# Optimization experiments

Measured on AMD Instinct MI355X. Metric: run time of the kernel, lower is better.

## Reference

```python
import jax, jax.numpy as jnp
import numpy as np

D_MODEL = 1024
NUM_HEADS = 16
D_K = D_MODEL // NUM_HEADS
D_FF = 4096
EPS = 1e-5


def setup_inputs() -> dict:
    key = jax.random.key(0)
    ks = jax.random.split(key, 16)
    B, S = 2, 2048
    s_attn = 1.0 / np.sqrt(D_MODEL)
    s_ff1 = 1.0 / np.sqrt(D_MODEL)
    s_ff2 = 1.0 / np.sqrt(D_FF)
    return {
        "x": jax.random.normal(ks[0], (B, S, D_MODEL), jnp.float32),
        "Wq": jax.random.normal(ks[1], (D_MODEL, D_MODEL), jnp.float32) * s_attn,
        "bq": jnp.zeros((D_MODEL,), jnp.float32),
        "Wk": jax.random.normal(ks[2], (D_MODEL, D_MODEL), jnp.float32) * s_attn,
        "bk": jnp.zeros((D_MODEL,), jnp.float32),
        "Wv": jax.random.normal(ks[3], (D_MODEL, D_MODEL), jnp.float32) * s_attn,
        "bv": jnp.zeros((D_MODEL,), jnp.float32),
        "Wo": jax.random.normal(ks[4], (D_MODEL, D_MODEL), jnp.float32) * s_attn,
        "bo": jnp.zeros((D_MODEL,), jnp.float32),
        "W1": jax.random.normal(ks[5], (D_MODEL, D_FF), jnp.float32) * s_ff1,
        "b1": jnp.zeros((D_FF,), jnp.float32),
        "W2": jax.random.normal(ks[6], (D_FF, D_MODEL), jnp.float32) * s_ff2,
        "b2": jnp.zeros((D_MODEL,), jnp.float32),
        "g1": jnp.ones((D_MODEL,), jnp.float32),
        "be1": jnp.zeros((D_MODEL,), jnp.float32),
        "g2": jnp.ones((D_MODEL,), jnp.float32),
        "be2": jnp.zeros((D_MODEL,), jnp.float32),
    }


def _layernorm(x, g, b):
    m = jnp.mean(x, axis=-1, keepdims=True)
    v = jnp.mean(jnp.square(x - m), axis=-1, keepdims=True)
    return (x - m) * jax.lax.rsqrt(v + EPS) * g + b


def _split_heads(x, B, S):
    # (B, S, D) -> (B, H, S, d_k)
    return x.reshape(B, S, NUM_HEADS, D_K).transpose(0, 2, 1, 3)


def reference(x, Wq, bq, Wk, bk, Wv, bv, Wo, bo, W1, b1, W2, b2, g1, be1, g2, be2):
    B, S, _ = x.shape
    Q = _split_heads(x @ Wq + bq, B, S)
    K = _split_heads(x @ Wk + bk, B, S)
    V = _split_heads(x @ Wv + bv, B, S)
    scores = jnp.einsum("bhqd,bhkd->bhqk", Q, K) / np.sqrt(D_K).astype(np.float32)
    attn = jax.nn.softmax(scores, axis=-1)  # dropout is identity (p=0 / eval)
    ctx = jnp.einsum("bhqk,bhkd->bhqd", attn, V)
    ctx = ctx.transpose(0, 2, 1, 3).reshape(B, S, D_MODEL)
    attn_out = ctx @ Wo + bo
    h = _layernorm(x + attn_out, g1, be1)
    ff = jax.nn.relu(h @ W1 + b1) @ W2 + b2
    out = _layernorm(h + ff, g2, be2)
    return out, attn
```

## Files before the change

kernel.cpp:

```cpp
#include <hip/hip_runtime.h>
#include <cstddef>
#include <cstdint>

#define D_MODEL 1024
#define NUM_HEADS 16
#define DK 64
#define D_FF 4096
#define SEQ 2048
#define BATCH 2
#define EPS 1e-5f

typedef unsigned short u16;
typedef __attribute__((ext_vector_type(8))) short bf16x8;
typedef __attribute__((ext_vector_type(8))) unsigned short us8;
typedef __attribute__((ext_vector_type(4))) unsigned short us4;
typedef __attribute__((ext_vector_type(4))) float f32x4;

#define SBAR() asm volatile("s_barrier" ::: "memory")

__device__ __forceinline__ u16 f2b(float f) {
    unsigned u = __float_as_uint(f);
    u += 0x7fffu + ((u >> 16) & 1u);
    return (u16)(u >> 16);
}
__device__ __forceinline__ float b2f(u16 v) {
    return __uint_as_float((unsigned)v << 16);
}

__device__ __forceinline__ void gload16(const void* g, void* l) {
    __builtin_amdgcn_global_load_lds(
        (const __attribute__((address_space(1))) void*)g,
        (__attribute__((address_space(3))) void*)l, 16, 0, 0);
}

__device__ __forceinline__ void stage_half(
    const u16* __restrict__ g, int ld, long kbase, int h,
    u16* dst, int tid, int wid)
{
#pragma unroll
    for (int r = 0; r < 2; ++r) {
        const int ci  = r * 512 + tid;
        const int row = ci >> 2;
        const int wd  = ci & 3;
        const int f   = (row + (row >> 2)) & 3;
        const long src = (long)row * ld + kbase + (long)(h * 4 + (wd ^ f)) * 8;
        gload16(g + src, dst + (r * 512 + wid * 64) * 8);
    }
}

__device__ __forceinline__ bf16x8 frag64(const u16* base, int ks, int row, int g) {
    const int f = (row + (row >> 2)) & 3;
    return *(const bf16x8*)&base[ks * 8192 + row * 32 + ((g ^ f) * 8)];
}

template<int KTOT, bool RELU>
__global__ __launch_bounds__(512, 2) void gemm256(
    const u16* __restrict__ Abf, const u16* __restrict__ BT,
    const float* __restrict__ bias0, u16* __restrict__ C0,
    int ldc, int nx)
{
    constexpr int NT = KTOT / 64;
    __shared__ u16 lds[2][32768];

    const int tid = threadIdx.x;
    const int wid = tid >> 6, l = tid & 63;
    const int r16 = l & 15, g = l >> 4;
    const int wr = wid >> 2, wc = wid & 3;

    const int nwg = gridDim.x;
    const int q = nwg >> 3, rr = nwg & 7;
    const int xcd = blockIdx.x & 7, idx = blockIdx.x >> 3;
    const int wg = (xcd < rr ? xcd * (q + 1) : rr * (q + 1) + (xcd - rr) * q) + idx;
    const long bm = (long)(wg / nx) * 256;
    const long bn = (long)(wg % nx) * 256;

    const u16* Ag = Abf + bm * KTOT;
    const u16* Bg = BT + bn * KTOT;

    f32x4 acc[8][4];
#pragma unroll
    for (int i = 0; i < 8; ++i)
#pragma unroll
        for (int n = 0; n < 4; ++n)
            acc[i][n] = (f32x4){0.f, 0.f, 0.f, 0.f};

    stage_half(Ag, KTOT, 0, 0, &lds[0][0],     tid, wid);
    stage_half(Ag, KTOT, 0, 1, &lds[0][8192],  tid, wid);
    stage_half(Bg, KTOT, 0, 0, &lds[0][16384], tid, wid);
    stage_half(Bg, KTOT, 0, 1, &lds[0][24576], tid, wid);
    if (NT > 1) {
        stage_half(Ag, KTOT, 64, 0, &lds[1][0],     tid, wid);
        stage_half(Bg, KTOT, 64, 0, &lds[1][16384], tid, wid);
    }
    asm volatile("s_waitcnt vmcnt(4)" ::: "memory");
    SBAR();

    for (int t = 0; t < NT; ++t) {
        u16* cur = &lds[t & 1][0];
        u16* nxt = &lds[(t + 1) & 1][0];
        const long k1 = (long)(t + 1) * 64;
        const long k2 = (long)(t + 2) * 64;
        const bool s1 = (t + 1 < NT), s2 = (t + 2 < NT);

        bf16x8 a0[4], b0[4];
#pragma unroll
        for (int i = 0; i < 4; ++i) {
            a0[i] = frag64(cur,         0, wr * 128 + i * 16 + r16, g);
            b0[i] = frag64(cur + 16384, 0, wc * 64  + i * 16 + r16, g);
        }
        if (s1) stage_half(Ag, KTOT, k1, 1, nxt + 8192, tid, wid);
        SBAR();
        __builtin_amdgcn_s_setprio(1);
#pragma unroll
        for (int i = 0; i < 4; ++i)
#pragma unroll
            for (int n = 0; n < 4; ++n)
                acc[i][n] = __builtin_amdgcn_mfma_f32_16x16x32_bf16(
                    a0[i], b0[n], acc[i][n], 0, 0, 0);
        __builtin_amdgcn_s_setprio(0);
        SBAR();

        bf16x8 a1[4];
#pragma unroll
        for (int i = 0; i < 4; ++i)
            a1[i] = frag64(cur, 0, wr * 128 + (i + 4) * 16 + r16, g);
        if (s1) stage_half(Bg, KTOT, k1, 1, nxt + 24576, tid, wid);
        SBAR();
        __builtin_amdgcn_s_setprio(1);
#pragma unroll
        for (int i = 0; i < 4; ++i)
#pragma unroll
            for (int n = 0; n < 4; ++n)
                acc[i + 4][n] = __builtin_amdgcn_mfma_f32_16x16x32_bf16(
                    a1[i], b0[n], acc[i + 4][n], 0, 0, 0);
        __builtin_amdgcn_s_setprio(0);
        SBAR();

        bf16x8 a2[4], b1[4];
#pragma unroll
        for (int i = 0; i < 4; ++i) {
            a2[i] = frag64(cur,         1, wr * 128 + i * 16 + r16, g);
            b1[i] = frag64(cur + 16384, 1, wc * 64  + i * 16 + r16, g);
        }
        if (s2) stage_half(Ag, KTOT, k2, 0, cur, tid, wid);
        SBAR();
        __builtin_amdgcn_s_setprio(1);
#pragma unroll
        for (int i = 0; i < 4; ++i)
#pragma unroll
            for (int n = 0; n < 4; ++n)
                acc[i][n] = __builtin_amdgcn_mfma_f32_16x16x32_bf16(
                    a2[i], b1[n], acc[i][n], 0, 0, 0);
        __builtin_amdgcn_s_setprio(0);
        SBAR();

        bf16x8 a3[4];
#pragma unroll
        for (int i = 0; i < 4; ++i)
            a3[i] = frag64(cur, 1, wr * 128 + (i + 4) * 16 + r16, g);
        if (s2) stage_half(Bg, KTOT, k2, 0, cur + 16384, tid, wid);
        SBAR();
        __builtin_amdgcn_s_setprio(1);
#pragma unroll
        for (int i = 0; i < 4; ++i)
#pragma unroll
            for (int n = 0; n < 4; ++n)
                acc[i + 4][n] = __builtin_amdgcn_mfma_f32_16x16x32_bf16(
                    a3[i], b1[n], acc[i + 4][n], 0, 0, 0);
        __builtin_amdgcn_s_setprio(0);
        if (s2)      asm volatile("s_waitcnt vmcnt(4)" ::: "memory");
        else if (s1) asm volatile("s_waitcnt vmcnt(0)" ::: "memory");
        SBAR();
    }

    const long crow0 = bm + wr * 128 + g * 4;
    const long ccol0 = bn + wc * 64 + r16;
#pragma unroll
    for (int n = 0; n < 4; ++n) {
        const long col = ccol0 + n * 16;
        const float bv = bias0[col];
#pragma unroll
        for (int i = 0; i < 8; ++i)
#pragma unroll
            for (int j = 0; j < 4; ++j) {
                const long row = crow0 + i * 16 + j;
                float v = acc[i][n][j] + bv;
                if (RELU) v = fmaxf(v, 0.f);
                C0[row * (long)ldc + col] = f2b(v);
            }
    }
}

template<bool RELU, int NSPLIT>
__global__ __launch_bounds__(256) void gemm_mfma(
    const u16* __restrict__ Abf, const u16* __restrict__ BT,
    const float* __restrict__ bias0, const float* __restrict__ bias1,
    const float* __restrict__ bias2,
    u16* __restrict__ C0, u16* __restrict__ C1, u16* __restrict__ C2,
    int lda, int ldb, int ldc, int K, int nx)
{
    constexpr int BM = 128, BN = 128;
    constexpr int MI = 4, NI = 4;
    constexpr int RA = 2, RB = 2;
    constexpr int TILE = (BM + BN) * 32;

    __shared__ u16 sm[3][TILE];

    const int tid = threadIdx.x;
    const int w = tid >> 6, l = tid & 63;
    const int r16 = l & 15, g = l >> 4;
    const int wr = w >> 1, wc = w & 1;

    const int nwg = gridDim.x;
    const int q = nwg >> 3, rr = nwg & 7;
    const int xcd = blockIdx.x & 7, idx = blockIdx.x >> 3;
    const int wg = (xcd < rr ? xcd * (q + 1) : rr * (q + 1) + (xcd - rr) * q) + idx;
    const long bm = (long)(wg / nx) * BM;
    const long bn = (long)(wg % nx) * BN;

    f32x4 acc[MI][NI];
#pragma unroll
    for (int mi = 0; mi < MI; ++mi)
#pragma unroll
        for (int ni = 0; ni < NI; ++ni)
            acc[mi][ni] = (f32x4){0.f, 0.f, 0.f, 0.f};

    long aOff[RA], bOff[RB];
#pragma unroll
    for (int r = 0; r < RA; ++r) {
        int c = r * 256 + tid;
        aOff[r] = (long)(bm + (c >> 2)) * lda + (c & 3) * 8;
    }
#pragma unroll
    for (int r = 0; r < RB; ++r) {
        int c = r * 256 + tid;
        bOff[r] = (long)(bn + (c >> 2)) * ldb + (c & 3) * 8;
    }

#pragma unroll
    for (int r = 0; r < RA; ++r)
        gload16(Abf + aOff[r], &sm[0][0] + (r * 256 + w * 64) * 8);
#pragma unroll
    for (int r = 0; r < RB; ++r)
        gload16(BT + bOff[r], &sm[0][BM * 32] + (r * 256 + w * 64) * 8);
    if (K > 32) {
#pragma unroll
        for (int r = 0; r < RA; ++r)
            gload16(Abf + aOff[r] + 32, &sm[1][0] + (r * 256 + w * 64) * 8);
#pragma unroll
        for (int r = 0; r < RB; ++r)
            gload16(BT + bOff[r] + 32, &sm[1][BM * 32] + (r * 256 + w * 64) * 8);
    }
    asm volatile("s_waitcnt vmcnt(4)" ::: "memory");
    SBAR();

    int cur = 0;
    for (int k0 = 0; k0 < K; k0 += 32) {
        const int nx2 = (cur >= 1) ? cur - 1 : cur + 2;
        if (k0 + 64 < K) {
#pragma unroll
            for (int r = 0; r < RA; ++r)
                gload16(Abf + aOff[r] + k0 + 64, &sm[nx2][0] + (r * 256 + w * 64) * 8);
#pragma unroll
            for (int r = 0; r < RB; ++r)
                gload16(BT + bOff[r] + k0 + 64, &sm[nx2][BM * 32] + (r * 256 + w * 64) * 8);
        }

        const u16* smA = &sm[cur][0];
        const u16* smB = &sm[cur][BM * 32];
        bf16x8 af[MI], bfr[NI];
#pragma unroll
        for (int mi = 0; mi < MI; ++mi)
            af[mi] = *(const bf16x8*)&smA[(wr * 64 + mi * 16 + r16) * 32 + g * 8];
#pragma unroll
        for (int ni = 0; ni < NI; ++ni)
            bfr[ni] = *(const bf16x8*)&smB[(wc * 64 + ni * 16 + r16) * 32 + g * 8];
#pragma unroll
        for (int mi = 0; mi < MI; ++mi)
#pragma unroll
            for (int ni = 0; ni < NI; ++ni)
                acc[mi][ni] = __builtin_amdgcn_mfma_f32_16x16x32_bf16(
                    af[mi], bfr[ni], acc[mi][ni], 0, 0, 0);

        if (k0 + 64 < K)      asm volatile("s_waitcnt vmcnt(4)" ::: "memory");
        else if (k0 + 32 < K) asm volatile("s_waitcnt vmcnt(0)" ::: "memory");
        SBAR();
        cur = (cur == 2) ? 0 : cur + 1;
    }

    u16* Cb = C0; const float* bp = bias0; long coff = 0;
    if (NSPLIT == 3) {
        const int grp = (int)(bn >> 10);
        if (grp == 1)      { Cb = C1; bp = bias1; }
        else if (grp == 2) { Cb = C2; bp = bias2; }
        coff = (long)grp << 10;
    }
    const long crow0 = bm + wr * 64 + g * 4;
    const long ccol0 = bn + wc * 64 + r16 - coff;
#pragma unroll
    for (int ni = 0; ni < NI; ++ni) {
        const long col = ccol0 + ni * 16;
        const float bv = bp[col];
#pragma unroll
        for (int mi = 0; mi < MI; ++mi) {
#pragma unroll
            for (int j = 0; j < 4; ++j) {
                const long row = crow0 + mi * 16 + j;
                float v = acc[mi][ni][j] + bv;
                if (RELU) v = fmaxf(v, 0.f);
                Cb[row * (long)ldc + col] = f2b(v);
            }
        }
    }
}

template<bool RELU>
__global__ __launch_bounds__(256) void gemm_n64(
    const u16* __restrict__ Abf, const u16* __restrict__ BT,
    const float* __restrict__ bias, u16* __restrict__ C,
    int lda, int ldb, int ldc, int K, int nx)
{
    constexpr int BM = 128, BN = 64;
    constexpr int MI = 2, NI = 4;
    constexpr int RA = 2, RB = 1;
    constexpr int TILE = (BM + BN) * 32;

    __shared__ u16 sm[3][TILE];

    const int tid = threadIdx.x;
    const int w = tid >> 6, l = tid & 63;
    const int r16 = l & 15, g = l >> 4;

    const int nwg = gridDim.x;
    const int q = nwg >> 3, rr = nwg & 7;
    const int xcd = blockIdx.x & 7, idx = blockIdx.x >> 3;
    const int wg = (xcd < rr ? xcd * (q + 1) : rr * (q + 1) + (xcd - rr) * q) + idx;
    const long bm = (long)(wg / nx) * BM;
    const long bn = (long)(wg % nx) * BN;

    f32x4 acc[MI][NI];
#pragma unroll
    for (int mi = 0; mi < MI; ++mi)
#pragma unroll
        for (int ni = 0; ni < NI; ++ni)
            acc[mi][ni] = (f32x4){0.f, 0.f, 0.f, 0.f};

    long aOff[RA], bOff[RB];
#pragma unroll
    for (int r = 0; r < RA; ++r) {
        int c = r * 256 + tid;
        aOff[r] = (long)(bm + (c >> 2)) * lda + (c & 3) * 8;
    }
#pragma unroll
    for (int r = 0; r < RB; ++r) {
        int c = r * 256 + tid;
        bOff[r] = (long)(bn + (c >> 2)) * ldb + (c & 3) * 8;
    }

#pragma unroll
    for (int r = 0; r < RA; ++r)
        gload16(Abf + aOff[r], &sm[0][0] + (r * 256 + w * 64) * 8);
#pragma unroll
    for (int r = 0; r < RB; ++r)
        gload16(BT + bOff[r], &sm[0][BM * 32] + (r * 256 + w * 64) * 8);
    if (K > 32) {
#pragma unroll
        for (int r = 0; r < RA; ++r)
            gload16(Abf + aOff[r] + 32, &sm[1][0] + (r * 256 + w * 64) * 8);
#pragma unroll
        for (int r = 0; r < RB; ++r)
            gload16(BT + bOff[r] + 32, &sm[1][BM * 32] + (r * 256 + w * 64) * 8);
    }
    asm volatile("s_waitcnt vmcnt(3)" ::: "memory");
    SBAR();

    int cur = 0;
    for (int k0 = 0; k0 < K; k0 += 32) {
        const int nx2 = (cur >= 1) ? cur - 1 : cur + 2;
        if (k0 + 64 < K) {
#pragma unroll
            for (int r = 0; r < RA; ++r)
                gload16(Abf + aOff[r] + k0 + 64, &sm[nx2][0] + (r * 256 + w * 64) * 8);
#pragma unroll
            for (int r = 0; r < RB; ++r)
                gload16(BT + bOff[r] + k0 + 64, &sm[nx2][BM * 32] + (r * 256 + w * 64) * 8);
        }

        const u16* smA = &sm[cur][0];
        const u16* smB = &sm[cur][BM * 32];
        bf16x8 af[MI], bfr[NI];
#pragma unroll
        for (int mi = 0; mi < MI; ++mi)
            af[mi] = *(const bf16x8*)&smA[(w * 32 + mi * 16 + r16) * 32 + g * 8];
#pragma unroll
        for (int ni = 0; ni < NI; ++ni)
            bfr[ni] = *(const bf16x8*)&smB[(ni * 16 + r16) * 32 + g * 8];
#pragma unroll
        for (int mi = 0; mi < MI; ++mi)
#pragma unroll
            for (int ni = 0; ni < NI; ++ni)
                acc[mi][ni] = __builtin_amdgcn_mfma_f32_16x16x32_bf16(
                    af[mi], bfr[ni], acc[mi][ni], 0, 0, 0);

        if (k0 + 64 < K)      asm volatile("s_waitcnt vmcnt(3)" ::: "memory");
        else if (k0 + 32 < K) asm volatile("s_waitcnt vmcnt(0)" ::: "memory");
        SBAR();
        cur = (cur == 2) ? 0 : cur + 1;
    }

    const long crow0 = bm + w * 32 + g * 4;
    const long ccol0 = bn + r16;
#pragma unroll
    for (int ni = 0; ni < NI; ++ni) {
        const long col = ccol0 + ni * 16;
        const float bv = bias[col];
#pragma unroll
        for (int mi = 0; mi < MI; ++mi) {
#pragma unroll
            for (int j = 0; j < 4; ++j) {
                const long row = crow0 + mi * 16 + j;
                float v = acc[mi][ni][j] + bv;
                if (RELU) v = fmaxf(v, 0.f);
                C[row * (long)ldc + col] = f2b(v);
            }
        }
    }
}

#define QBLK 128
#define KBLK 64
#define NTT (SEQ / KBLK)
#define C2E 0.18033688f

__global__ __launch_bounds__(256) void flash_attn(
    const u16* __restrict__ Qg, const u16* __restrict__ Kg,
    const u16* __restrict__ Vt, float* __restrict__ attn,
    u16* __restrict__ ctx)
{
    __shared__ u16 smem[16384];
    __shared__ u16 Ps[4][2048];

    u16* const Qs  = smem;
    u16* const kb0 = smem + 8192;
    u16* const kb1 = smem;

    const int tid = threadIdx.x;
    const int w = tid >> 6, l = tid & 63;
    const int r16 = l & 15, g = l >> 4;

    const int wg = (blockIdx.x & 7) * (gridDim.x >> 3) + (blockIdx.x >> 3);
    const int qb = wg & 15, z = wg >> 4;
    const int b = z >> 4, h = z & 15;
    const long q0 = (long)qb * QBLK;

    const long kBase = ((long)b * SEQ) * D_MODEL + h * DK;
    const long vBase = (long)z * DK * SEQ;

#pragma unroll
    for (int r = 0; r < 4; ++r) {
        int c = r * 256 + tid;
        int row = c >> 3, bl = c & 7;
        long src = ((long)b * SEQ + q0 + row) * D_MODEL + h * DK
                 + ((bl ^ (row & 7)) * 8);
        gload16(Qg + src, Qs + (r * 256 + w * 64) * 8);
    }
#pragma unroll
    for (int r = 0; r < 2; ++r) {
        int c = r * 256 + tid;
        int row = c >> 3, bl = c & 7;
        gload16(Kg + kBase + (long)row * D_MODEL + ((bl ^ (row & 7)) * 8),
                kb0 + (r * 256 + w * 64) * 8);
    }
    __syncthreads();

    bf16x8 qf[2][2];
#pragma unroll
    for (int qi = 0; qi < 2; ++qi)
#pragma unroll
        for (int ks = 0; ks < 2; ++ks)
            qf[qi][ks] = *(const bf16x8*)
                &Qs[(w * 32 + qi * 16 + r16) * 64 + (((ks * 4 + g) ^ (r16 & 7)) * 8)];
    __syncthreads();

    float lrun[2] = {0.f, 0.f};

    for (int t = 0; t < NTT; ++t) {
        if (t + 1 < NTT) {
            u16* kdst = ((t + 1) & 1) ? kb1 : kb0;
            const long kro = (long)(t + 1) * KBLK;
#pragma unroll
            for (int r = 0; r < 2; ++r) {
                int c = r * 256 + tid;
                int row = c >> 3, bl = c & 7;
                gload16(Kg + kBase + (kro + row) * D_MODEL + ((bl ^ (row & 7)) * 8),
                        kdst + (r * 256 + w * 64) * 8);
            }
        }
        const u16* kcur = (t & 1) ? kb1 : kb0;

        f32x4 sT[4][2];
#pragma unroll
        for (int ki = 0; ki < 4; ++ki)
#pragma unroll
            for (int qi = 0; qi < 2; ++qi) sT[ki][qi] = (f32x4){0.f, 0.f, 0.f, 0.f};

        __builtin_amdgcn_s_setprio(1);
#pragma unroll
        for (int ks = 0; ks < 2; ++ks) {
            bf16x8 kf[4];
#pragma unroll
            for (int ki = 0; ki < 4; ++ki)
                kf[ki] = *(const bf16x8*)
                    &kcur[(ki * 16 + r16) * 64 + (((ks * 4 + g) ^ (r16 & 7)) * 8)];
#pragma unroll
            for (int ki = 0; ki < 4; ++ki)
#pragma unroll
                for (int qi = 0; qi < 2; ++qi)
                    sT[ki][qi] = __builtin_amdgcn_mfma_f32_16x16x32_bf16(
                        kf[ki], qf[qi][ks], sT[ki][qi], 0, 0, 0);
        }
        __builtin_amdgcn_s_setprio(0);

#pragma unroll
        for (int qi = 0; qi < 2; ++qi) {
            float ls = 0.f;
#pragma unroll
            for (int ki = 0; ki < 4; ++ki)
#pragma unroll
                for (int j = 0; j < 4; ++j)
                    ls += exp2f(sT[ki][qi][j] * C2E);
            ls += __shfl_xor(ls, 16);
            ls += __shfl_xor(ls, 32);
            lrun[qi] += ls;
        }
        __syncthreads();
    }

    const float il[2] = {1.0f / lrun[0], 1.0f / lrun[1]};

    u16* const p2b0 = smem + 8192;
    u16* const p2b1 = smem;
#pragma unroll
    for (int r = 0; r < 2; ++r) {
        int c = r * 256 + tid;
        int row = c >> 3, bl = c & 7;
        gload16(Kg + kBase + (long)row * D_MODEL + ((bl ^ (row & 7)) * 8),
                p2b0 + (r * 256 + w * 64) * 8);
        gload16(Vt + vBase + (long)row * SEQ + ((bl ^ (row & 7)) * 8),
                p2b0 + 4096 + (r * 256 + w * 64) * 8);
    }
    __syncthreads();

    f32x4 acc2[2][4];
#pragma unroll
    for (int mi = 0; mi < 2; ++mi)
#pragma unroll
        for (int ni = 0; ni < 4; ++ni) acc2[mi][ni] = (f32x4){0.f, 0.f, 0.f, 0.f};

    const long arow0 = ((long)z * SEQ + q0 + w * 32) * (long)SEQ;

    for (int t = 0; t < NTT; ++t) {
        const int k0 = t * KBLK;
        if (t + 1 < NTT) {
            u16* dst = ((t + 1) & 1) ? p2b1 : p2b0;
            const long kro = (long)(t + 1) * KBLK;
#pragma unroll
            for (int r = 0; r < 2; ++r) {
                int c = r * 256 + tid;
                int row = c >> 3, bl = c & 7;
                gload16(Kg + kBase + (kro + row) * D_MODEL + ((bl ^ (row & 7)) * 8),
                        dst + (r * 256 + w * 64) * 8);
                gload16(Vt + vBase + (long)row * SEQ + kro + ((bl ^ (row & 7)) * 8),
                        dst + 4096 + (r * 256 + w * 64) * 8);
            }
        }
        const u16* kcur = (t & 1) ? p2b1 : p2b0;
        const u16* vcur = kcur + 4096;

        f32x4 sT[4][2];
#pragma unroll
        for (int ki = 0; ki < 4; ++ki)
#pragma unroll
            for (int qi = 0; qi < 2; ++qi) sT[ki][qi] = (f32x4){0.f, 0.f, 0.f, 0.f};

        __builtin_amdgcn_s_setprio(1);
#pragma unroll
        for (int ks = 0; ks < 2; ++ks) {
            bf16x8 kf[4];
#pragma unroll
            for (int ki = 0; ki < 4; ++ki)
                kf[ki] = *(const bf16x8*)
                    &kcur[(ki * 16 + r16) * 64 + (((ks * 4 + g) ^ (r16 & 7)) * 8)];
#pragma unroll
            for (int ki = 0; ki < 4; ++ki)
#pragma unroll
                for (int qi = 0; qi < 2; ++qi)
                    sT[ki][qi] = __builtin_amdgcn_mfma_f32_16x16x32_bf16(
                        kf[ki], qf[qi][ks], sT[ki][qi], 0, 0, 0);
        }
        __builtin_amdgcn_s_setprio(0);

#pragma unroll
        for (int qi = 0; qi < 2; ++qi) {
            const long ar = arow0 + (long)(qi * 16 + r16) * SEQ + k0 + g * 4;
            const int prow = (qi * 16 + r16) * 64;
#pragma unroll
            for (int ki = 0; ki < 4; ++ki) {
                f32x4 p;
                p[0] = exp2f(sT[ki][qi][0] * C2E) * il[qi];
                p[1] = exp2f(sT[ki][qi][1] * C2E) * il[qi];
                p[2] = exp2f(sT[ki][qi][2] * C2E) * il[qi];
                p[3] = exp2f(sT[ki][qi][3] * C2E) * il[qi];
                __builtin_nontemporal_store(p, (f32x4*)&attn[ar + ki * 16]);
                us4 pb;
                pb[0] = f2b(p[0]); pb[1] = f2b(p[1]);
                pb[2] = f2b(p[2]); pb[3] = f2b(p[3]);
                const int kblk = 2 * ki + (g >> 1);
                *(us4*)&Ps[w][prow + ((kblk ^ (r16 & 7)) << 3) + ((g & 1) << 2)] = pb;
            }
        }

        __builtin_amdgcn_s_setprio(1);
#pragma unroll
        for (int ks = 0; ks < 2; ++ks) {
            bf16x8 pf[2], vf[4];
#pragma unroll
            for (int mi = 0; mi < 2; ++mi)
                pf[mi] = *(const bf16x8*)
                    &Ps[w][(mi * 16 + r16) * 64 + (((ks * 4 + g) ^ (r16 & 7)) << 3)];
#pragma unroll
            for (int ni = 0; ni < 4; ++ni)
                vf[ni] = *(const bf16x8*)
                    &vcur[(ni * 16 + r16) * 64 + (((ks * 4 + g) ^ (r16 & 7)) * 8)];
#pragma unroll
            for (int mi = 0; mi < 2; ++mi)
#pragma unroll
                for (int ni = 0; ni < 4; ++ni)
                    acc2[mi][ni] = __builtin_amdgcn_mfma_f32_16x16x32_bf16(
                        pf[mi], vf[ni], acc2[mi][ni], 0, 0, 0);
        }
        __builtin_amdgcn_s_setprio(0);

        if (t + 1 < NTT) {
            asm volatile("s_waitcnt vmcnt(8)" ::: "memory");
            SBAR();
        }
    }

#pragma unroll
    for (int mi = 0; mi < 2; ++mi)
#pragma unroll
        for (int j = 0; j < 4; ++j) {
            const long grow = (long)b * SEQ + q0 + w * 32 + mi * 16 + g * 4 + j;
#pragma unroll
            for (int ni = 0; ni < 4; ++ni)
                ctx[grow * D_MODEL + h * DK + ni * 16 + r16] = f2b(acc2[mi][ni][j]);
        }
}

__device__ __forceinline__ void tr32(
    const float* __restrict__ W, u16* __restrict__ Wt, int R, int C,
    int bx, int by, int tx, int ty, float (*t)[33])
{
    const long c = (long)bx * 32 + tx;
    const long r0 = (long)by * 32;
#pragma unroll
    for (int j = 0; j < 32; j += 8)
        t[ty + j][tx] = W[(r0 + ty + j) * C + c];
    __syncthreads();
    const long r = r0 + tx;
#pragma unroll
    for (int j = 0; j < 32; j += 8)
        Wt[((long)bx * 32 + ty + j) * R + r] = f2b(t[tx][ty + j]);
}

__global__ __launch_bounds__(256) void preproc(
    const float* __restrict__ x, u16* __restrict__ x_bf,
    const float* __restrict__ Wq, const float* __restrict__ Wk,
    const float* __restrict__ Wv, const float* __restrict__ Wo,
    u16* __restrict__ Wqkvo_t,
    const float* __restrict__ W1, u16* __restrict__ W1t,
    const float* __restrict__ W2, u16* __restrict__ W2t)
{
    __shared__ float t[32][33];
    int bid = blockIdx.x;
    const int tx = threadIdx.x & 31, ty = threadIdx.x >> 5;

    if (bid < 2048) {
        long i = ((long)bid * 256 + threadIdx.x) * 8;
        float4 a = *(const float4*)(x + i);
        float4 b = *(const float4*)(x + i + 4);
        us8 o;
        o[0] = f2b(a.x); o[1] = f2b(a.y); o[2] = f2b(a.z); o[3] = f2b(a.w);
        o[4] = f2b(b.x); o[5] = f2b(b.y); o[6] = f2b(b.z); o[7] = f2b(b.w);
        *(us8*)(x_bf + i) = o;
        return;
    }
    bid -= 2048;
    if (bid < 4096) {
        const int z = bid >> 10, rem = bid & 1023;
        const float* W = (z == 0) ? Wq : (z == 1) ? Wk : (z == 2) ? Wv : Wo;
        tr32(W, Wqkvo_t + (size_t)z * D_MODEL * D_MODEL, D_MODEL, D_MODEL,
             rem & 31, rem >> 5, tx, ty, t);
        return;
    }
    bid -= 4096;
    if (bid < 4096) {
        tr32(W1, W1t, D_MODEL, D_FF, bid & 127, bid >> 7, tx, ty, t);
        return;
    }
    bid -= 4096;
    {
        tr32(W2, W2t, D_FF, D_MODEL, bid & 31, bid >> 5, tx, ty, t);
    }
}

__global__ __launch_bounds__(256) void transpose_v(
    const u16* __restrict__ V, u16* __restrict__ Vt)
{
    __shared__ u16 t[32][33];
    const int z = blockIdx.z, b = z >> 4, h = z & 15;
    const int tx = threadIdx.x & 31, ty = threadIdx.x >> 5;
    const long k0 = (long)blockIdx.x * 32;
    const long d0 = (long)blockIdx.y * 32;
#pragma unroll
    for (int j = 0; j < 32; j += 8)
        t[ty + j][tx] = V[((long)b * SEQ + k0 + ty + j) * D_MODEL + h * DK + d0 + tx];
    __syncthreads();
#pragma unroll
    for (int j = 0; j < 32; j += 8)
        Vt[((long)z * DK + d0 + ty + j) * SEQ + k0 + tx] = t[tx][ty + j];
}

template<int OM>
__global__ __launch_bounds__(256) void add_ln_kernel(
    const u16* __restrict__ a, const u16* __restrict__ b,
    const float* __restrict__ g, const float* __restrict__ be,
    void* __restrict__ outp)
{
    const int l = threadIdx.x & 63, w = threadIdx.x >> 6;
    const long row = (long)blockIdx.x * 4 + w;
    const long base = row * D_MODEL;

    float xv[16];
#pragma unroll
    for (int c = 0; c < 2; ++c) {
        const long off = c * 512 + l * 8;
        us8 av = *(const us8*)(a + base + off);
        us8 bv = *(const us8*)(b + base + off);
#pragma unroll
        for (int i = 0; i < 8; ++i)
            xv[c * 8 + i] = b2f(av[i]) + b2f(bv[i]);
    }

    float s = 0.f;
#pragma unroll
    for (int i = 0; i < 16; ++i) s += xv[i];
#pragma unroll
    for (int off = 1; off < 64; off <<= 1) s += __shfl_xor(s, off);
    const float mean = s * (1.0f / D_MODEL);

    float ss = 0.f;
#pragma unroll
    for (int i = 0; i < 16; ++i) {
        xv[i] -= mean;
        ss += xv[i] * xv[i];
    }
#pragma unroll
    for (int off = 1; off < 64; off <<= 1) ss += __shfl_xor(ss, off);
    const float rs = rsqrtf(ss * (1.0f / D_MODEL) + EPS);

#pragma unroll
    for (int c = 0; c < 2; ++c) {
        const long off = c * 512 + l * 8;
        float4 g0 = *(const float4*)(g + off);
        float4 g1 = *(const float4*)(g + off + 4);
        float4 b0 = *(const float4*)(be + off);
        float4 b1 = *(const float4*)(be + off + 4);
        float o[8];
        o[0] = xv[c*8+0] * rs * g0.x + b0.x;
        o[1] = xv[c*8+1] * rs * g0.y + b0.y;
        o[2] = xv[c*8+2] * rs * g0.z + b0.z;
        o[3] = xv[c*8+3] * rs * g0.w + b0.w;
        o[4] = xv[c*8+4] * rs * g1.x + b1.x;
        o[5] = xv[c*8+5] * rs * g1.y + b1.y;
        o[6] = xv[c*8+6] * rs * g1.z + b1.z;
        o[7] = xv[c*8+7] * rs * g1.w + b1.w;
        if (OM == 0) {
            float4 v0 = {o[0], o[1], o[2], o[3]};
            float4 v1 = {o[4], o[5], o[6], o[7]};
            *(float4*)((float*)outp + base + off) = v0;
            *(float4*)((float*)outp + base + off + 4) = v1;
        } else {
            us8 ob;
#pragma unroll
            for (int i = 0; i < 8; ++i) ob[i] = f2b(o[i]);
            *(us8*)((u16*)outp + base + off) = ob;
        }
    }
}

extern "C" void kernel_launch(void* const* d_in, const int* in_sizes, int n_in,
                              void* d_out, int out_size, void* d_ws, size_t ws_size,
                              hipStream_t stream)
{
    const float* x   = (const float*)d_in[0];
    const float* Wq  = (const float*)d_in[1];
    const float* bq  = (const float*)d_in[2];
    const float* Wk  = (const float*)d_in[3];
    const float* bk  = (const float*)d_in[4];
    const float* Wv  = (const float*)d_in[5];
    const float* bv  = (const float*)d_in[6];
    const float* Wo  = (const float*)d_in[7];
    const float* bo  = (const float*)d_in[8];
    const float* W1  = (const float*)d_in[9];
    const float* b1  = (const float*)d_in[10];
    const float* W2  = (const float*)d_in[11];
    const float* b2  = (const float*)d_in[12];
    const float* g1  = (const float*)d_in[13];
    const float* be1 = (const float*)d_in[14];
    const float* g2  = (const float*)d_in[15];
    const float* be2 = (const float*)d_in[16];

    float* out  = (float*)d_out;
    float* attn = out + (size_t)BATCH * SEQ * D_MODEL;

    char* ws = (char*)d_ws;
    const size_t MB = 1u << 20;
    u16* x_bf    = (u16*)(ws);
    u16* Q_bf    = (u16*)(ws + 8 * MB);
    u16* K_bf    = (u16*)(ws + 16 * MB);
    u16* Vt      = (u16*)(ws + 24 * MB);
    u16* V_bf    = (u16*)(ws + 32 * MB);
    u16* Wqkvo_t = (u16*)(ws + 40 * MB);
    u16* W1t     = (u16*)(ws + 48 * MB);
    u16* W2t     = (u16*)(ws + 56 * MB);
    u16* ff1_bf  = (u16*)(ws + 64 * MB);
    u16* ctx_bf  = (u16*)(ws + 96 * MB);
    u16* Wot     = Wqkvo_t + (size_t)3 * D_MODEL * D_MODEL;
    u16* h_bf    = K_bf;
    u16* ao_bf   = V_bf;
    u16* ff2_bf  = Vt;

    const int M = BATCH * SEQ;
    dim3 T(256);

    preproc<<<dim3(2048 + 3 * 4096), T, 0, stream>>>(
        x, x_bf, Wq, Wk, Wv, Wo, Wqkvo_t, W1, W1t, W2, W2t);

    gemm_mfma<false, 3><<<dim3((M / 128) * 24), T, 0, stream>>>(
        x_bf, Wqkvo_t, bq, bk, bv, Q_bf, K_bf, V_bf,
        D_MODEL, D_MODEL, D_MODEL, D_MODEL, 24);

    transpose_v<<<dim3(SEQ / 32, DK / 32, BATCH * NUM_HEADS), T, 0, stream>>>(V_bf, Vt);

    flash_attn<<<dim3((SEQ / QBLK) * BATCH * NUM_HEADS), T, 0, stream>>>(
        Q_bf, K_bf, Vt, attn, ctx_bf);

    gemm_n64<false><<<dim3((M / 128) * 16), T, 0, stream>>>(
        ctx_bf, Wot, bo, ao_bf, D_MODEL, D_MODEL, D_MODEL, D_MODEL, 16);

    add_ln_kernel<1><<<dim3(M / 4), T, 0, stream>>>(x_bf, ao_bf, g1, be1, h_bf);

    gemm256<D_MODEL, true><<<dim3((M / 256) * (D_FF / 256)), dim3(512), 0, stream>>>(
        h_bf, W1t, b1, ff1_bf, D_FF, D_FF / 256);

    gemm_n64<false><<<dim3((M / 128) * 16), T, 0, stream>>>(
        ff1_bf, W2t, b2, ff2_bf, D_FF, D_FF, D_MODEL, D_FF, 16);

    add_ln_kernel<0><<<dim3(M / 4), T, 0, stream>>>(h_bf, ff2_bf, g2, be2, out);
}
```

Before: 399.0 us.

## Deepen GEMM K-step to 64 with swizzled LDS and widen attention key blocks

The N=64 GEMM now stages 64-wide K slices with an XOR-swizzled LDS layout, so each barrier covers two MFMA k-steps. MFMA issue is also wrapped in setprio. The flash attention kernel moves from 64-key to 128-key blocks. Its first pass (softmax denominator) uses a 3-buffer prefetch two tiles ahead, and its second pass processes two 64-key sub-tiles per barrier with a 16-way swizzled V layout. Together these halve the barrier and wait count per unit of work, at the cost of more LDS per block, which may lower occupancy.

```diff
diff --git a/kernel.cpp b/kernel.cpp
--- a/kernel.cpp
+++ b/kernel.cpp
@@ -320,11 +320,7 @@
     const float* __restrict__ bias, u16* __restrict__ C,
     int lda, int ldb, int ldc, int K, int nx)
 {
-    constexpr int BM = 128, BN = 64;
-    constexpr int MI = 2, NI = 4;
-    constexpr int RA = 2, RB = 1;
-    constexpr int TILE = (BM + BN) * 32;
-
+    constexpr int TILE = 12288;
     __shared__ u16 sm[3][TILE];
 
     const int tid = threadIdx.x;
@@ -335,87 +331,88 @@
     const int q = nwg >> 3, rr = nwg & 7;
     const int xcd = blockIdx.x & 7, idx = blockIdx.x >> 3;
     const int wg = (xcd < rr ? xcd * (q + 1) : rr * (q + 1) + (xcd - rr) * q) + idx;
-    const long bm = (long)(wg / nx) * BM;
-    const long bn = (long)(wg % nx) * BN;
-
-    f32x4 acc[MI][NI];
-#pragma unroll
-    for (int mi = 0; mi < MI; ++mi)
-#pragma unroll
-        for (int ni = 0; ni < NI; ++ni)
+    const long bm = (long)(wg / nx) * 128;
+    const long bn = (long)(wg % nx) * 64;
+
+    f32x4 acc[2][4];
+#pragma unroll
+    for (int mi = 0; mi < 2; ++mi)
+#pragma unroll
+        for (int ni = 0; ni < 4; ++ni)
             acc[mi][ni] = (f32x4){0.f, 0.f, 0.f, 0.f};
 
-    long aOff[RA], bOff[RB];
-#pragma unroll
-    for (int r = 0; r < RA; ++r) {
+    long aOff[4], bOff[2];
+#pragma unroll
+    for (int r = 0; r < 4; ++r) {
         int c = r * 256 + tid;
-        aOff[r] = (long)(bm + (c >> 2)) * lda + (c & 3) * 8;
-    }
-#pragma unroll
-    for (int r = 0; r < RB; ++r) {
+        int row = c >> 3, sl = c & 7;
+        aOff[r] = (long)(bm + row) * lda + (long)(sl ^ (row & 7)) * 8;
+    }
+#pragma unroll
+    for (int r = 0; r < 2; ++r) {
         int c = r * 256 + tid;
-        bOff[r] = (long)(bn + (c >> 2)) * ldb + (c & 3) * 8;
-    }
-
-#pragma unroll
-    for (int r = 0; r < RA; ++r)
-        gload16(Abf + aOff[r], &sm[0][0] + (r * 256 + w * 64) * 8);
-#pragma unroll
-    for (int r = 0; r < RB; ++r)
-        gload16(BT + bOff[r], &sm[0][BM * 32] + (r * 256 + w * 64) * 8);
-    if (K > 32) {
-#pragma unroll
-        for (int r = 0; r < RA; ++r)
-            gload16(Abf + aOff[r] + 32, &sm[1][0] + (r * 256 + w * 64) * 8);
-#pragma unroll
-        for (int r = 0; r < RB; ++r)
-            gload16(BT + bOff[r] + 32, &sm[1][BM * 32] + (r * 256 + w * 64) * 8);
-    }
-    asm volatile("s_waitcnt vmcnt(3)" ::: "memory");
+        int row = c >> 3, sl = c & 7;
+        bOff[r] = (long)(bn + row) * ldb + (long)(sl ^ (row & 7)) * 8;
+    }
+
+#define N64_STAGE(buf, koff)                                                  \
+    {                                                                         \
+        _Pragma("unroll")                                                     \
+        for (int r = 0; r < 4; ++r)                                           \
+            gload16(Abf + aOff[r] + (koff), &sm[buf][0] + (r * 256 + w * 64) * 8); \
+        _Pragma("unroll")                                                     \
+        for (int r = 0; r < 2; ++r)                                           \
+            gload16(BT + bOff[r] + (koff), &sm[buf][8192] + (r * 256 + w * 64) * 8); \
+    }
+
+    N64_STAGE(0, 0)
+    if (K > 64) N64_STAGE(1, 64)
+    asm volatile("s_waitcnt vmcnt(6)" ::: "memory");
     SBAR();
 
     int cur = 0;
-    for (int k0 = 0; k0 < K; k0 += 32) {
+    for (int k0 = 0; k0 < K; k0 += 64) {
         const int nx2 = (cur >= 1) ? cur - 1 : cur + 2;
-        if (k0 + 64 < K) {
-#pragma unroll
-            for (int r = 0; r < RA; ++r)
-                gload16(Abf + aOff[r] + k0 + 64, &sm[nx2][0] + (r * 256 + w * 64) * 8);
-#pragma unroll
-            for (int r = 0; r < RB; ++r)
-                gload16(BT + bOff[r] + k0 + 64, &sm[nx2][BM * 32] + (r * 256 + w * 64) * 8);
-        }
+        if (k0 + 128 < K) N64_STAGE(nx2, k0 + 128)
 
         const u16* smA = &sm[cur][0];
-        const u16* smB = &sm[cur][BM * 32];
-        bf16x8 af[MI], bfr[NI];
-#pragma unroll
-        for (int mi = 0; mi < MI; ++mi)
-            af[mi] = *(const bf16x8*)&smA[(w * 32 + mi * 16 + r16) * 32 + g * 8];
-#pragma unroll
-        for (int ni = 0; ni < NI; ++ni)
-            bfr[ni] = *(const bf16x8*)&smB[(ni * 16 + r16) * 32 + g * 8];
-#pragma unroll
-        for (int mi = 0; mi < MI; ++mi)
-#pragma unroll
-            for (int ni = 0; ni < NI; ++ni)
-                acc[mi][ni] = __builtin_amdgcn_mfma_f32_16x16x32_bf16(
-                    af[mi], bfr[ni], acc[mi][ni], 0, 0, 0);
-
-        if (k0 + 64 < K)      asm volatile("s_waitcnt vmcnt(3)" ::: "memory");
-        else if (k0 + 32 < K) asm volatile("s_waitcnt vmcnt(0)" ::: "memory");
+        const u16* smB = &sm[cur][8192];
+#pragma unroll
+        for (int ks = 0; ks < 2; ++ks) {
+            bf16x8 af[2], bfr[4];
+#pragma unroll
+            for (int mi = 0; mi < 2; ++mi)
+                af[mi] = *(const bf16x8*)
+                    &smA[(w * 32 + mi * 16 + r16) * 64 + (((ks * 4 + g) ^ (r16 & 7)) * 8)];
+#pragma unroll
+            for (int ni = 0; ni < 4; ++ni)
+                bfr[ni] = *(const bf16x8*)
+                    &smB[(ni * 16 + r16) * 64 + (((ks * 4 + g) ^ (r16 & 7)) * 8)];
+            __builtin_amdgcn_s_setprio(1);
+#pragma unroll
+            for (int mi = 0; mi < 2; ++mi)
+#pragma unroll
+                for (int ni = 0; ni < 4; ++ni)
+                    acc[mi][ni] = __builtin_amdgcn_mfma_f32_16x16x32_bf16(
+                        af[mi], bfr[ni], acc[mi][ni], 0, 0, 0);
+            __builtin_amdgcn_s_setprio(0);
+        }
+
+        if (k0 + 128 < K)      asm volatile("s_waitcnt vmcnt(6)" ::: "memory");
+        else if (k0 + 64 < K)  asm volatile("s_waitcnt vmcnt(0)" ::: "memory");
         SBAR();
         cur = (cur == 2) ? 0 : cur + 1;
     }
+#undef N64_STAGE
 
     const long crow0 = bm + w * 32 + g * 4;
     const long ccol0 = bn + r16;
 #pragma unroll
-    for (int ni = 0; ni < NI; ++ni) {
+    for (int ni = 0; ni < 4; ++ni) {
         const long col = ccol0 + ni * 16;
         const float bv = bias[col];
 #pragma unroll
-        for (int mi = 0; mi < MI; ++mi) {
+        for (int mi = 0; mi < 2; ++mi) {
 #pragma unroll
             for (int j = 0; j < 4; ++j) {
                 const long row = crow0 + mi * 16 + j;
@@ -428,8 +425,8 @@
 }
 
 #define QBLK 128
-#define KBLK 64
-#define NTT (SEQ / KBLK)
+#define KB2 128
+#define NT2 (SEQ / KB2)
 #define C2E 0.18033688f
 
 __global__ __launch_bounds__(256) void flash_attn(
@@ -437,12 +434,8 @@
     const u16* __restrict__ Vt, float* __restrict__ attn,
     u16* __restrict__ ctx)
 {
-    __shared__ u16 smem[16384];
+    __shared__ u16 smem[32768];
     __shared__ u16 Ps[4][2048];
-
-    u16* const Qs  = smem;
-    u16* const kb0 = smem + 8192;
-    u16* const kb1 = smem;
 
     const int tid = threadIdx.x;
     const int w = tid >> 6, l = tid & 63;
@@ -456,21 +449,38 @@
     const long kBase = ((long)b * SEQ) * D_MODEL + h * DK;
     const long vBase = (long)z * DK * SEQ;
 
+    u16* const Qs = smem + 24576;
+
 #pragma unroll
     for (int r = 0; r < 4; ++r) {
         int c = r * 256 + tid;
         int row = c >> 3, bl = c & 7;
-        long src = ((long)b * SEQ + q0 + row) * D_MODEL + h * DK
-                 + ((bl ^ (row & 7)) * 8);
-        gload16(Qg + src, Qs + (r * 256 + w * 64) * 8);
-    }
-#pragma unroll
-    for (int r = 0; r < 2; ++r) {
-        int c = r * 256 + tid;
-        int row = c >> 3, bl = c & 7;
-        gload16(Kg + kBase + (long)row * D_MODEL + ((bl ^ (row & 7)) * 8),
-                kb0 + (r * 256 + w * 64) * 8);
-    }
+        gload16(Qg + ((long)b * SEQ + q0 + row) * D_MODEL + h * DK + ((bl ^ (row & 7)) * 8),
+                Qs + (r * 256 + w * 64) * 8);
+    }
+#define STAGE_K(dst, kro)                                                     \
+    {                                                                         \
+        _Pragma("unroll")                                                     \
+        for (int r = 0; r < 4; ++r) {                                         \
+            int c = r * 256 + tid;                                            \
+            int row = c >> 3, bl = c & 7;                                     \
+            gload16(Kg + kBase + ((kro) + row) * (long)D_MODEL + ((bl ^ (row & 7)) * 8), \
+                    (dst) + (r * 256 + w * 64) * 8);                          \
+        }                                                                     \
+    }
+#define STAGE_V(dst, kro)                                                     \
+    {                                                                         \
+        _Pragma("unroll")                                                     \
+        for (int r = 0; r < 4; ++r) {                                         \
+            int c = r * 256 + tid;                                            \
+            int row = c >> 4, bl = c & 15;                                    \
+            gload16(Vt + vBase + (long)row * SEQ + (kro) + ((bl ^ (row & 15)) * 8), \
+                    (dst) + (r * 256 + w * 64) * 8);                          \
+        }                                                                     \
+    }
+
+    STAGE_K(smem, 0)
+    STAGE_K(smem + 16384, KB2)
     __syncthreads();
 
     bf16x8 qf[2][2];
@@ -484,168 +494,158 @@
 
     float lrun[2] = {0.f, 0.f};
 
-    for (int t = 0; t < NTT; ++t) {
-        if (t + 1 < NTT) {
-            u16* kdst = ((t + 1) & 1) ? kb1 : kb0;
-            const long kro = (long)(t + 1) * KBLK;
-#pragma unroll
-            for (int r = 0; r < 2; ++r) {
-                int c = r * 256 + tid;
-                int row = c >> 3, bl = c & 7;
-                gload16(Kg + kBase + (kro + row) * D_MODEL + ((bl ^ (row & 7)) * 8),
-                        kdst + (r * 256 + w * 64) * 8);
+    for (int t = 0; t < NT2; ++t) {
+        const int m3n = (t + 2) % 3;
+        u16* kdst = (m3n == 0) ? smem : (m3n == 1) ? smem + 16384 : smem + 8192;
+        if (t + 2 < NT2) STAGE_K(kdst, (long)(t + 2) * KB2)
+        const int m3c = t % 3;
+        const u16* kcur = (m3c == 0) ? smem : (m3c == 1) ? smem + 16384 : smem + 8192;
+
+#pragma unroll
+        for (int sub = 0; sub < 2; ++sub) {
+            f32x4 sT[4][2];
+#pragma unroll
+            for (int ki = 0; ki < 4; ++ki)
+#pragma unroll
+                for (int qi = 0; qi < 2; ++qi) sT[ki][qi] = (f32x4){0.f, 0.f, 0.f, 0.f};
+
+            __builtin_amdgcn_s_setprio(1);
+#pragma unroll
+            for (int ks = 0; ks < 2; ++ks) {
+                bf16x8 kf[4];
+#pragma unroll
+                for (int ki = 0; ki < 4; ++ki)
+                    kf[ki] = *(const bf16x8*)
+                        &kcur[(sub * 64 + ki * 16 + r16) * 64 + (((ks * 4 + g) ^ (r16 & 7)) * 8)];
+#pragma unroll
+                for (int ki = 0; ki < 4; ++ki)
+#pragma unroll
+                    for (int qi = 0; qi < 2; ++qi)
+                        sT[ki][qi] = __builtin_amdgcn_mfma_f32_16x16x32_bf16(
+                            kf[ki], qf[qi][ks], sT[ki][qi], 0, 0, 0);
             }
-        }
-        const u16* kcur = (t & 1) ? kb1 : kb0;
-
-        f32x4 sT[4][2];
-#pragma unroll
-        for (int ki = 0; ki < 4; ++ki)
-#pragma unroll
-            for (int qi = 0; qi < 2; ++qi) sT[ki][qi] = (f32x4){0.f, 0.f, 0.f, 0.f};
-
-        __builtin_amdgcn_s_setprio(1);
-#pragma unroll
-        for (int ks = 0; ks < 2; ++ks) {
-            bf16x8 kf[4];
+            __builtin_amdgcn_s_setprio(0);
+
+#pragma unroll
+            for (int qi = 0; qi < 2; ++qi) {
+                float ls = 0.f;
+#pragma unroll
+                for (int ki = 0; ki < 4; ++ki)
+#pragma unroll
+                    for (int j = 0; j < 4; ++j)
+                        ls += exp2f(sT[ki][qi][j] * C2E);
+                ls += __shfl_xor(ls, 16);
+                ls += __shfl_xor(ls, 32);
+                lrun[qi] += ls;
+            }
+        }
+        if (t + 2 < NT2)      asm volatile("s_waitcnt vmcnt(4)" ::: "memory");
+        else if (t + 1 < NT2) asm volatile("s_waitcnt vmcnt(0)" ::: "memory");
+        if (t + 1 < NT2) SBAR();
+    }
+
+    const float il[2] = {1.0f / lrun[0], 1.0f / lrun[1]};
+
+    __syncthreads();
+    STAGE_K(smem, 0)
+    STAGE_V(smem + 8192, 0)
+    __syncthreads();
+
+    f32x4 acc2[2][4];
+#pragma unroll
+    for (int mi = 0; mi < 2; ++mi)
+#pragma unroll
+        for (int ni = 0; ni < 4; ++ni) acc2[mi][ni] = (f32x4){0.f, 0.f, 0.f, 0.f};
+
+    const long arow0 = ((long)z * SEQ + q0 + w * 32) * (long)SEQ;
+
+    for (int t = 0; t < NT2; ++t) {
+        const int k0 = t * KB2;
+        if (t + 1 < NT2) {
+            u16* dst = smem + ((t + 1) & 1) * 16384;
+            STAGE_K(dst, (long)(t + 1) * KB2)
+            STAGE_V(dst + 8192, (long)(t + 1) * KB2)
+        }
+        const u16* kcur = smem + (t & 1) * 16384;
+        const u16* vcur = kcur + 8192;
+
+#pragma unroll
+        for (int sub = 0; sub < 2; ++sub) {
+            f32x4 sT[4][2];
 #pragma unroll
             for (int ki = 0; ki < 4; ++ki)
-                kf[ki] = *(const bf16x8*)
-                    &kcur[(ki * 16 + r16) * 64 + (((ks * 4 + g) ^ (r16 & 7)) * 8)];
-#pragma unroll
-            for (int ki = 0; ki < 4; ++ki)
-#pragma unroll
-                for (int qi = 0; qi < 2; ++qi)
-                    sT[ki][qi] = __builtin_amdgcn_mfma_f32_16x16x32_bf16(
-                        kf[ki], qf[qi][ks], sT[ki][qi], 0, 0, 0);
-        }
-        __builtin_amdgcn_s_setprio(0);
-
-#pragma unroll
-        for (int qi = 0; qi < 2; ++qi) {
-            float ls = 0.f;
-#pragma unroll
-            for (int ki = 0; ki < 4; ++ki)
-#pragma unroll
-                for (int j = 0; j < 4; ++j)
-                    ls += exp2f(sT[ki][qi][j] * C2E);
-            ls += __shfl_xor(ls, 16);
-            ls += __shfl_xor(ls, 32);
-            lrun[qi] += ls;
-        }
-        __syncthreads();
-    }
-
-    const float il[2] = {1.0f / lrun[0], 1.0f / lrun[1]};
-
-    u16* const p2b0 = smem + 8192;
-    u16* const p2b1 = smem;
-#pragma unroll
-    for (int r = 0; r < 2; ++r) {
-        int c = r * 256 + tid;
-        int row = c >> 3, bl = c & 7;
-        gload16(Kg + kBase + (long)row * D_MODEL + ((bl ^ (row & 7)) * 8),
-                p2b0 + (r * 256 + w * 64) * 8);
-        gload16(Vt + vBase + (long)row * SEQ + ((bl ^ (row & 7)) * 8),
-                p2b0 + 4096 + (r * 256 + w * 64) * 8);
-    }
-    __syncthreads();
-
-    f32x4 acc2[2][4];
-#pragma unroll
-    for (int mi = 0; mi < 2; ++mi)
-#pragma unroll
-        for (int ni = 0; ni < 4; ++ni) acc2[mi][ni] = (f32x4){0.f, 0.f, 0.f, 0.f};
-
-    const long arow0 = ((long)z * SEQ + q0 + w * 32) * (long)SEQ;
-
-    for (int t = 0; t < NTT; ++t) {
-        const int k0 = t * KBLK;
-        if (t + 1 < NTT) {
-            u16* dst = ((t + 1) & 1) ? p2b1 : p2b0;
-            const long kro = (long)(t + 1) * KBLK;
-#pragma unroll
-            for (int r = 0; r < 2; ++r) {
-                int c = r * 256 + tid;
-                int row = c >> 3, bl = c & 7;
-                gload16(Kg + kBase + (kro + row) * D_MODEL + ((bl ^ (row & 7)) * 8),
-                        dst + (r * 256 + w * 64) * 8);
-                gload16(Vt + vBase + (long)row * SEQ + kro + ((bl ^ (row & 7)) * 8),
-                        dst + 4096 + (r * 256 + w * 64) * 8);
+#pragma unroll
+                for (int qi = 0; qi < 2; ++qi) sT[ki][qi] = (f32x4){0.f, 0.f, 0.f, 0.f};
+
+            __builtin_amdgcn_s_setprio(1);
+#pragma unroll
+            for (int ks = 0; ks < 2; ++ks) {
+                bf16x8 kf[4];
+#pragma unroll
+                for (int ki = 0; ki < 4; ++ki)
+                    kf[ki] = *(const bf16x8*)
+                        &kcur[(sub * 64 + ki * 16 + r16) * 64 + (((ks * 4 + g) ^ (r16 & 7)) * 8)];
+#pragma unroll
+                for (int ki = 0; ki < 4; ++ki)
+#pragma unroll
+                    for (int qi = 0; qi < 2; ++qi)
+                        sT[ki][qi] = __builtin_amdgcn_mfma_f32_16x16x32_bf16(
+                            kf[ki], qf[qi][ks], sT[ki][qi], 0, 0, 0);
             }
-        }
-        const u16* kcur = (t & 1) ? p2b1 : p2b0;
-        const u16* vcur = kcur + 4096;
-
-        f32x4 sT[4][2];
-#pragma unroll
-        for (int ki = 0; ki < 4; ++ki)
-#pragma unroll
-            for (int qi = 0; qi < 2; ++qi) sT[ki][qi] = (f32x4){0.f, 0.f, 0.f, 0.f};
-
-        __builtin_amdgcn_s_setprio(1);
-#pragma unroll
-        for (int ks = 0; ks < 2; ++ks) {
-            bf16x8 kf[4];
-#pragma unroll
-            for (int ki = 0; ki < 4; ++ki)
-                kf[ki] = *(const bf16x8*)
-                    &kcur[(ki * 16 + r16) * 64 + (((ks * 4 + g) ^ (r16 & 7)) * 8)];
-#pragma unroll
-            for (int ki = 0; ki < 4; ++ki)
-#pragma unroll
-                for (int qi = 0; qi < 2; ++qi)
-                    sT[ki][qi] = __builtin_amdgcn_mfma_f32_16x16x32_bf16(
-                        kf[ki], qf[qi][ks], sT[ki][qi], 0, 0, 0);
-        }
-        __builtin_amdgcn_s_setprio(0);
-
-#pragma unroll
-        for (int qi = 0; qi < 2; ++qi) {
-            const long ar = arow0 + (long)(qi * 16 + r16) * SEQ + k0 + g * 4;
-            const int prow = (qi * 16 + r16) * 64;
-#pragma unroll
-            for (int ki = 0; ki < 4; ++ki) {
-                f32x4 p;
-                p[0] = exp2f(sT[ki][qi][0] * C2E) * il[qi];
-                p[1] = exp2f(sT[ki][qi][1] * C2E) * il[qi];
-                p[2] = exp2f(sT[ki][qi][2] * C2E) * il[qi];
-                p[3] = exp2f(sT[ki][qi][3] * C2E) * il[qi];
-                __builtin_nontemporal_store(p, (f32x4*)&attn[ar + ki * 16]);
-                us4 pb;
-                pb[0] = f2b(p[0]); pb[1] = f2b(p[1]);
-                pb[2] = f2b(p[2]); pb[3] = f2b(p[3]);
-                const int kblk = 2 * ki + (g >> 1);
-                *(us4*)&Ps[w][prow + ((kblk ^ (r16 & 7)) << 3) + ((g & 1) << 2)] = pb;
+            __builtin_amdgcn_s_setprio(0);
+
+#pragma unroll
+            for (int qi = 0; qi < 2; ++qi) {
+                const long ar = arow0 + (long)(qi * 16 + r16) * SEQ + k0 + sub * 64 + g * 4;
+                const int prow = (qi * 16 + r16) * 64;
+#pragma unroll
+                for (int ki = 0; ki < 4; ++ki) {
+                    f32x4 p;
+                    p[0] = exp2f(sT[ki][qi][0] * C2E) * il[qi];
+                    p[1] = exp2f(sT[ki][qi][1] * C2E) * il[qi];
+                    p[2] = exp2f(sT[ki][qi][2] * C2E) * il[qi];
+                    p[3] = exp2f(sT[ki][qi][3] * C2E) * il[qi];
+                    __builtin_nontemporal_store(p, (f32x4*)&attn[ar + ki * 16]);
+                    us4 pb;
+                    pb[0] = f2b(p[0]); pb[1] = f2b(p[1]);
+                    pb[2] = f2b(p[2]); pb[3] = f2b(p[3]);
+                    const int kblk = 2 * ki + (g >> 1);
+                    *(us4*)&Ps[w][prow + ((kblk ^ (r16 & 7)) << 3) + ((g & 1) << 2)] = pb;
+                }
             }
-        }
-
-        __builtin_amdgcn_s_setprio(1);
-#pragma unroll
-        for (int ks = 0; ks < 2; ++ks) {
-            bf16x8 pf[2], vf[4];
-#pragma unroll
-            for (int mi = 0; mi < 2; ++mi)
-                pf[mi] = *(const bf16x8*)
-                    &Ps[w][(mi * 16 + r16) * 64 + (((ks * 4 + g) ^ (r16 & 7)) << 3)];
-#pragma unroll
-            for (int ni = 0; ni < 4; ++ni)
-                vf[ni] = *(const bf16x8*)
-                    &vcur[(ni * 16 + r16) * 64 + (((ks * 4 + g) ^ (r16 & 7)) * 8)];
-#pragma unroll
-            for (int mi = 0; mi < 2; ++mi)
-#pragma unroll
-                for (int ni = 0; ni < 4; ++ni)
-                    acc2[mi][ni] = __builtin_amdgcn_mfma_f32_16x16x32_bf16(
-                        pf[mi], vf[ni], acc2[mi][ni], 0, 0, 0);
-        }
-        __builtin_amdgcn_s_setprio(0);
-
-        if (t + 1 < NTT) {
-            asm volatile("s_waitcnt vmcnt(8)" ::: "memory");
+
+            __builtin_amdgcn_s_setprio(1);
+#pragma unroll
+            for (int ks = 0; ks < 2; ++ks) {
+                bf16x8 pf[2], vf[4];
+#pragma unroll
+                for (int mi = 0; mi < 2; ++mi)
+                    pf[mi] = *(const bf16x8*)
+                        &Ps[w][(mi * 16 + r16) * 64 + (((ks * 4 + g) ^ (r16 & 7)) << 3)];
+#pragma unroll
+                for (int ni = 0; ni < 4; ++ni) {
+                    const int row = ni * 16 + r16;
+                    const int slot = sub * 8 + ks * 4 + g;
+                    vf[ni] = *(const bf16x8*)
+                        &vcur[row * 128 + ((slot ^ (row & 15)) * 8)];
+                }
+#pragma unroll
+                for (int mi = 0; mi < 2; ++mi)
+#pragma unroll
+                    for (int ni = 0; ni < 4; ++ni)
+                        acc2[mi][ni] = __builtin_amdgcn_mfma_f32_16x16x32_bf16(
+                            pf[mi], vf[ni], acc2[mi][ni], 0, 0, 0);
+            }
+            __builtin_amdgcn_s_setprio(0);
+        }
+
+        if (t + 1 < NT2) {
+            asm volatile("s_waitcnt vmcnt(16)" ::: "memory");
             SBAR();
         }
     }
+#undef STAGE_K
+#undef STAGE_V
 
 #pragma unroll
     for (int mi = 0; mi < 2; ++mi)
```

New measurement: 384.6 us. 3.6% less time.
